# Kernel optimization log

Hardware: AMD Instinct MI355X
Metric: run time of the kernel (lower is better)

The kernel has to match this reference:

```python
import jax, jax.numpy as jnp
import numpy as np

N_SENT = 65536
N_BAGS = 4096
REL_DIM = 768
FLAT_C = 53
GLOBAL_C = 95


def setup_inputs() -> dict:
    key = jax.random.key(0)
    k1, k2, k3, k4, k5 = jax.random.split(key, 5)
    x = jax.random.normal(k1, (N_SENT, REL_DIM), dtype=jnp.float32)
    attention_query = jax.random.randint(k2, (N_SENT, 3), 0, GLOBAL_C, dtype=jnp.int32)
    # strictly increasing interior boundaries -> every bag non-empty
    rng = np.random.RandomState(0)
    interior = np.sort(rng.choice(np.arange(1, N_SENT), N_BAGS - 1, replace=False))
    scope = jnp.asarray(np.concatenate([[0], interior, [N_SENT]]), dtype=jnp.int32)
    # learned params (xavier-like scale for embeddings, normal bias)
    attention_weight = jax.random.normal(k3, (GLOBAL_C, REL_DIM), dtype=jnp.float32) * (2.0 / (GLOBAL_C + REL_DIM)) ** 0.5
    relation_weight = jax.random.normal(k4, (FLAT_C, REL_DIM * 3), dtype=jnp.float32) * (2.0 / (FLAT_C + REL_DIM * 3)) ** 0.5
    bias = jax.random.normal(k5, (FLAT_C,), dtype=jnp.float32)
    return {"x": x, "attention_query": attention_query, "scope": scope,
            "attention_weight": attention_weight, "relation_weight": relation_weight,
            "bias": bias}


def _segment_ids(scope, n):
    # scope: [B+1] offsets; build per-sentence bag id via boundary scatter + cumsum
    marks = jnp.zeros((n,), dtype=jnp.int32).at[scope[1:-1]].add(1)
    return jnp.cumsum(marks)


def reference(x, attention_query, scope, attention_weight, relation_weight, bias):
    n = x.shape[0]
    n_bags = scope.shape[0] - 1
    seg = _segment_ids(scope, n)  # [N]

    # per-layer attention logits: sum(x * attention_emb, -1) for all 3 layers at once
    att = attention_weight[attention_query]                # [N, 3, D]
    logit = jnp.einsum('nd,nld->nl', x, att)               # [N, 3]

    # segment (per-bag) softmax over sentences, per layer
    seg_max = jax.ops.segment_max(logit, seg, num_segments=n_bags)   # [B, 3]
    w = jnp.exp(logit - seg_max[seg])
    denom = jax.ops.segment_sum(w, seg, num_segments=n_bags)         # [B, 3]
    w = w / denom[seg]                                               # [N, 3]

    # weighted sentence aggregation per bag, per layer
    bag = jax.ops.segment_sum(w[:, :, None] * x[:, None, :], seg, num_segments=n_bags)  # [B, 3, D]

    stack_logits_layers = jnp.transpose(bag, (1, 0, 2))    # [3, B, D]
    logits_total = bag.reshape(n_bags, -1)                 # [B, 3*D] == cat(layer0, layer1, layer2)
    # dropout in eval mode (identity); global_ratio > 0 -> compute probs
    probs = logits_total @ relation_weight.T + bias        # [B, FLAT_C]
    return (stack_logits_layers, logits_total, probs)
```

## Files before the change

kernel.cpp:

```cpp
#include <hip/hip_runtime.h>
#include <math.h>

#define NSENT 65536
#define NBAGS 4096
#define DIM 768
#define D4 192
#define FLATC 53
#define CPAD 64
#define KTOT 2304
#define K4 576
#define CHUNK 512

typedef short bf16x8 __attribute__((ext_vector_type(8)));
typedef float f32x4 __attribute__((ext_vector_type(4)));

__device__ __forceinline__ float wsum(float v) {
#pragma unroll
  for (int o = 32; o; o >>= 1) v += __shfl_xor(v, o);
  return v;
}
__device__ __forceinline__ float wmax(float v) {
#pragma unroll
  for (int o = 32; o; o >>= 1) v = fmaxf(v, __shfl_xor(v, o));
  return v;
}
__device__ __forceinline__ float dot4(float4 a, float4 b) {
  return a.x * b.x + a.y * b.y + a.z * b.z + a.w * b.w;
}
__device__ __forceinline__ unsigned short f2bf(float f) {
  unsigned int u = __float_as_uint(f);
  return (unsigned short)((u + 0x7FFFu + ((u >> 16) & 1u)) >> 16);
}

__global__ __launch_bounds__(256) void logit_kernel(
    const float* __restrict__ x, const int* __restrict__ q,
    const float* __restrict__ aw, float* __restrict__ lgout) {
  const int wid = (blockIdx.x * 256 + threadIdx.x) >> 6;
  const int lane = threadIdx.x & 63;
  const int n0 = wid * 2;
  if (n0 >= NSENT) return;
  const int n1 = n0 + 1;

  const int qa0 = q[3 * n0 + 0], qa1 = q[3 * n0 + 1], qa2 = q[3 * n0 + 2];
  const int qb0 = q[3 * n1 + 0], qb1 = q[3 * n1 + 1], qb2 = q[3 * n1 + 2];

  const float4* __restrict__ X4 = (const float4*)x;
  const float4* __restrict__ AW4 = (const float4*)aw;
  const float4* xr0 = X4 + (size_t)n0 * D4;
  const float4* xr1 = X4 + (size_t)n1 * D4;
  const float4* A00 = AW4 + (size_t)qa0 * D4;
  const float4* A01 = AW4 + (size_t)qa1 * D4;
  const float4* A02 = AW4 + (size_t)qa2 * D4;
  const float4* A10 = AW4 + (size_t)qb0 * D4;
  const float4* A11 = AW4 + (size_t)qb1 * D4;
  const float4* A12 = AW4 + (size_t)qb2 * D4;

  float p00 = 0.f, p01 = 0.f, p02 = 0.f;
  float p10 = 0.f, p11 = 0.f, p12 = 0.f;
#pragma unroll
  for (int j = 0; j < 3; j++) {
    const int idx = lane + 64 * j;
    const float4 x0 = xr0[idx];
    const float4 x1 = xr1[idx];
    p00 += dot4(x0, A00[idx]);
    p01 += dot4(x0, A01[idx]);
    p02 += dot4(x0, A02[idx]);
    p10 += dot4(x1, A10[idx]);
    p11 += dot4(x1, A11[idx]);
    p12 += dot4(x1, A12[idx]);
  }
  p00 = wsum(p00); p01 = wsum(p01); p02 = wsum(p02);
  p10 = wsum(p10); p11 = wsum(p11); p12 = wsum(p12);
  if (lane == 0) {
    lgout[3 * n0 + 0] = p00;
    lgout[3 * n0 + 1] = p01;
    lgout[3 * n0 + 2] = p02;
    lgout[3 * n1 + 0] = p10;
    lgout[3 * n1 + 1] = p11;
    lgout[3 * n1 + 2] = p12;
  }
}

__global__ __launch_bounds__(192) void bag_sum(
    const float* __restrict__ x, const float* __restrict__ lgin,
    const int* __restrict__ scope, float* __restrict__ out,
    unsigned short* __restrict__ lt16) {
  const int b = blockIdx.x;
  const int s0 = scope[b];
  const int s1 = scope[b + 1];
  const int len = s1 - s0;
  const int tid = threadIdx.x;
  const int wave = tid >> 6;
  const int lane = tid & 63;

  __shared__ float lg[CHUNK][3];
  __shared__ float sm[3], se[3];

  float m[3] = {-INFINITY, -INFINITY, -INFINITY};
  float dsum[3] = {0.f, 0.f, 0.f};
  float4 acc[3];
#pragma unroll
  for (int l = 0; l < 3; l++) acc[l] = make_float4(0.f, 0.f, 0.f, 0.f);

  const float4* __restrict__ X4 = (const float4*)x;

  for (int cs = 0; cs < len; cs += CHUNK) {
    const int clen = min(CHUNK, len - cs);

    for (int idx = tid; idx < 3 * clen; idx += 192)
      ((float*)lg)[idx] = lgin[(size_t)(s0 + cs) * 3 + idx];
    __syncthreads();

    {
      const int l = wave;
      float cm = -INFINITY;
      for (int i = lane; i < clen; i += 64) cm = fmaxf(cm, lg[i][l]);
      cm = wmax(cm);
      const float mn = fmaxf(m[l], cm);
      float es = 0.f;
      for (int i = lane; i < clen; i += 64) {
        const float e = __expf(lg[i][l] - mn);
        es += e;
        lg[i][l] = e;
      }
      es = wsum(es);
      if (lane == 0) {
        sm[l] = mn;
        se[l] = es;
      }
    }
    __syncthreads();

#pragma unroll
    for (int l = 0; l < 3; l++) {
      const float mn = sm[l];
      const float sc = __expf(m[l] - mn);
      m[l] = mn;
      dsum[l] = dsum[l] * sc + se[l];
      acc[l].x *= sc; acc[l].y *= sc; acc[l].z *= sc; acc[l].w *= sc;
    }

    {
      int i = 0;
      for (; i + 4 <= clen; i += 4) {
        float4 xv[4];
        float w0[4], w1[4], w2[4];
#pragma unroll
        for (int j = 0; j < 4; j++) {
          xv[j] = X4[(size_t)(s0 + cs + i + j) * D4 + tid];
          w0[j] = lg[i + j][0];
          w1[j] = lg[i + j][1];
          w2[j] = lg[i + j][2];
        }
#pragma unroll
        for (int j = 0; j < 4; j++) {
          acc[0].x += w0[j] * xv[j].x; acc[0].y += w0[j] * xv[j].y;
          acc[0].z += w0[j] * xv[j].z; acc[0].w += w0[j] * xv[j].w;
          acc[1].x += w1[j] * xv[j].x; acc[1].y += w1[j] * xv[j].y;
          acc[1].z += w1[j] * xv[j].z; acc[1].w += w1[j] * xv[j].w;
          acc[2].x += w2[j] * xv[j].x; acc[2].y += w2[j] * xv[j].y;
          acc[2].z += w2[j] * xv[j].z; acc[2].w += w2[j] * xv[j].w;
        }
      }
      for (; i < clen; i++) {
        const float a0 = lg[i][0], a1 = lg[i][1], a2 = lg[i][2];
        const float4 xv = X4[(size_t)(s0 + cs + i) * D4 + tid];
        acc[0].x += a0 * xv.x; acc[0].y += a0 * xv.y; acc[0].z += a0 * xv.z; acc[0].w += a0 * xv.w;
        acc[1].x += a1 * xv.x; acc[1].y += a1 * xv.y; acc[1].z += a1 * xv.z; acc[1].w += a1 * xv.w;
        acc[2].x += a2 * xv.x; acc[2].y += a2 * xv.y; acc[2].z += a2 * xv.z; acc[2].w += a2 * xv.w;
      }
    }
    __syncthreads();
  }

  float4* o0 = (float4*)out;
  float4* o1 = (float4*)(out + (size_t)3 * NBAGS * DIM);
  ushort4* l16 = (ushort4*)(lt16 + (size_t)b * KTOT);
#pragma unroll
  for (int l = 0; l < 3; l++) {
    const float inv = (dsum[l] > 0.f) ? (1.f / dsum[l]) : 0.f;
    float4 v = acc[l];
    v.x *= inv; v.y *= inv; v.z *= inv; v.w *= inv;
    o0[((size_t)l * NBAGS + b) * D4 + tid] = v;
    o1[(size_t)b * K4 + l * D4 + tid] = v;
    ushort4 h;
    h.x = f2bf(v.x); h.y = f2bf(v.y); h.z = f2bf(v.z); h.w = f2bf(v.w);
    l16[l * D4 + tid] = h;
  }
}

__global__ __launch_bounds__(256) void rwcvt(const float* __restrict__ rw,
                                             unsigned short* __restrict__ rw16) {
  const int idx = blockIdx.x * 256 + threadIdx.x;
  if (idx < CPAD * KTOT) {
    const int row = idx / KTOT;
    const float v = (row < FLATC) ? rw[idx] : 0.f;
    rw16[idx] = f2bf(v);
  }
}

__global__ __launch_bounds__(256) void probs_mfma(
    const unsigned short* __restrict__ lt16,
    const unsigned short* __restrict__ rw16,
    const float* __restrict__ bias, float* __restrict__ outp) {
  const int wv = threadIdx.x >> 6;
  const int lane = threadIdx.x & 63;
  const int r = lane & 15;
  const int kg = lane >> 4;
  const int bagbase = blockIdx.x * 64 + wv * 16;

  f32x4 acc[4];
#pragma unroll
  for (int ct = 0; ct < 4; ct++) acc[ct] = (f32x4){0.f, 0.f, 0.f, 0.f};

  const unsigned short* ap = lt16 + (size_t)(bagbase + r) * KTOT + kg * 8;
  const unsigned short* bp[4];
#pragma unroll
  for (int ct = 0; ct < 4; ct++)
    bp[ct] = rw16 + (size_t)(ct * 16 + r) * KTOT + kg * 8;

  for (int k = 0; k < KTOT; k += 32) {
    const bf16x8 a = *(const bf16x8*)(ap + k);
#pragma unroll
    for (int ct = 0; ct < 4; ct++) {
      const bf16x8 bb = *(const bf16x8*)(bp[ct] + k);
      acc[ct] = __builtin_amdgcn_mfma_f32_16x16x32_bf16(a, bb, acc[ct], 0, 0, 0);
    }
  }

#pragma unroll
  for (int ct = 0; ct < 4; ct++) {
    const int col = ct * 16 + r;
    if (col < FLATC) {
      const float bv = bias[col];
#pragma unroll
      for (int reg = 0; reg < 4; reg++) {
        const int bag = bagbase + kg * 4 + reg;
        outp[(size_t)bag * FLATC + col] = acc[ct][reg] + bv;
      }
    }
  }
}

extern "C" void kernel_launch(void* const* d_in, const int* in_sizes, int n_in,
                              void* d_out, int out_size, void* d_ws,
                              size_t ws_size, hipStream_t stream) {
  const float* x = (const float*)d_in[0];
  const int* aq = (const int*)d_in[1];
  const int* scope = (const int*)d_in[2];
  const float* aw = (const float*)d_in[3];
  const float* rw = (const float*)d_in[4];
  const float* bias = (const float*)d_in[5];
  float* out = (float*)d_out;

  unsigned short* lt16 = (unsigned short*)d_ws;
  unsigned short* rw16 = lt16 + (size_t)NBAGS * KTOT;
  float* lgbuf = (float*)(rw16 + (size_t)CPAD * KTOT);

  hipLaunchKernelGGL(logit_kernel, dim3(NSENT / 2 / 4), dim3(256), 0, stream,
                     x, aq, aw, lgbuf);
  hipLaunchKernelGGL(bag_sum, dim3(NBAGS), dim3(192), 0, stream, x, lgbuf,
                     scope, out, lt16);
  hipLaunchKernelGGL(rwcvt, dim3((CPAD * KTOT + 255) / 256), dim3(256), 0,
                     stream, rw, rw16);

  float* probs = out + (size_t)3 * NBAGS * DIM + (size_t)NBAGS * KTOT;
  hipLaunchKernelGGL(probs_mfma, dim3(NBAGS / 64), dim3(256), 0, stream, lt16,
                     rw16, bias, probs);
}
```

Before: 162.0 us.

## Compute attention logits as dense bf16 MFMA GEMM against all classes, then gather

```diff
diff --git a/kernel.cpp b/kernel.cpp
--- a/kernel.cpp
+++ b/kernel.cpp
@@ -1,4 +1,5 @@
 #include <hip/hip_runtime.h>
+#include <hip/hip_bf16.h>
 #include <math.h>
 
 #define NSENT 65536
@@ -7,9 +8,11 @@
 #define D4 192
 #define FLATC 53
 #define CPAD 64
+#define GCLS 96
 #define KTOT 2304
 #define K4 576
 #define CHUNK 512
+#define MROWS 128
 
 typedef short bf16x8 __attribute__((ext_vector_type(8)));
 typedef float f32x4 __attribute__((ext_vector_type(4)));
@@ -24,67 +27,78 @@
   for (int o = 32; o; o >>= 1) v = fmaxf(v, __shfl_xor(v, o));
   return v;
 }
-__device__ __forceinline__ float dot4(float4 a, float4 b) {
-  return a.x * b.x + a.y * b.y + a.z * b.z + a.w * b.w;
-}
 __device__ __forceinline__ unsigned short f2bf(float f) {
-  unsigned int u = __float_as_uint(f);
-  return (unsigned short)((u + 0x7FFFu + ((u >> 16) & 1u)) >> 16);
-}
-
-__global__ __launch_bounds__(256) void logit_kernel(
-    const float* __restrict__ x, const int* __restrict__ q,
-    const float* __restrict__ aw, float* __restrict__ lgout) {
-  const int wid = (blockIdx.x * 256 + threadIdx.x) >> 6;
+  union { __hip_bfloat16 b; unsigned short s; } cv;
+  cv.b = __float2bfloat16(f);
+  return cv.s;
+}
+__device__ __forceinline__ bf16x8 cvt8(float4 lo, float4 hi) {
+  union { bf16x8 v; unsigned short s[8]; } u;
+  u.s[0] = f2bf(lo.x); u.s[1] = f2bf(lo.y); u.s[2] = f2bf(lo.z); u.s[3] = f2bf(lo.w);
+  u.s[4] = f2bf(hi.x); u.s[5] = f2bf(hi.y); u.s[6] = f2bf(hi.z); u.s[7] = f2bf(hi.w);
+  return u.v;
+}
+
+__global__ __launch_bounds__(256) void cvt_weights(
+    const float* __restrict__ aw, const float* __restrict__ rw,
+    unsigned short* __restrict__ aw16, unsigned short* __restrict__ rw16) {
+  const int idx = blockIdx.x * 256 + threadIdx.x;
+  const int NAW = GCLS * DIM;
+  if (idx < NAW) {
+    const int row = idx / DIM;
+    aw16[idx] = f2bf(row < 95 ? aw[idx] : 0.f);
+  } else if (idx < NAW + CPAD * KTOT) {
+    const int j = idx - NAW;
+    const int row = j / KTOT;
+    rw16[j] = f2bf(row < FLATC ? rw[j] : 0.f);
+  }
+}
+
+__global__ __launch_bounds__(256) void logit_gemm(
+    const float* __restrict__ x, const unsigned short* __restrict__ aw16,
+    float* __restrict__ L) {
+  const int wv = threadIdx.x >> 6;
   const int lane = threadIdx.x & 63;
-  const int n0 = wid * 2;
-  if (n0 >= NSENT) return;
-  const int n1 = n0 + 1;
-
-  const int qa0 = q[3 * n0 + 0], qa1 = q[3 * n0 + 1], qa2 = q[3 * n0 + 2];
-  const int qb0 = q[3 * n1 + 0], qb1 = q[3 * n1 + 1], qb2 = q[3 * n1 + 2];
-
-  const float4* __restrict__ X4 = (const float4*)x;
-  const float4* __restrict__ AW4 = (const float4*)aw;
-  const float4* xr0 = X4 + (size_t)n0 * D4;
-  const float4* xr1 = X4 + (size_t)n1 * D4;
-  const float4* A00 = AW4 + (size_t)qa0 * D4;
-  const float4* A01 = AW4 + (size_t)qa1 * D4;
-  const float4* A02 = AW4 + (size_t)qa2 * D4;
-  const float4* A10 = AW4 + (size_t)qb0 * D4;
-  const float4* A11 = AW4 + (size_t)qb1 * D4;
-  const float4* A12 = AW4 + (size_t)qb2 * D4;
-
-  float p00 = 0.f, p01 = 0.f, p02 = 0.f;
-  float p10 = 0.f, p11 = 0.f, p12 = 0.f;
-#pragma unroll
-  for (int j = 0; j < 3; j++) {
-    const int idx = lane + 64 * j;
-    const float4 x0 = xr0[idx];
-    const float4 x1 = xr1[idx];
-    p00 += dot4(x0, A00[idx]);
-    p01 += dot4(x0, A01[idx]);
-    p02 += dot4(x0, A02[idx]);
-    p10 += dot4(x1, A10[idx]);
-    p11 += dot4(x1, A11[idx]);
-    p12 += dot4(x1, A12[idx]);
-  }
-  p00 = wsum(p00); p01 = wsum(p01); p02 = wsum(p02);
-  p10 = wsum(p10); p11 = wsum(p11); p12 = wsum(p12);
-  if (lane == 0) {
-    lgout[3 * n0 + 0] = p00;
-    lgout[3 * n0 + 1] = p01;
-    lgout[3 * n0 + 2] = p02;
-    lgout[3 * n1 + 0] = p10;
-    lgout[3 * n1 + 1] = p11;
-    lgout[3 * n1 + 2] = p12;
-  }
+  const int r = lane & 15;
+  const int kg = lane >> 4;
+  const int m0 = blockIdx.x * MROWS + wv * 32;
+
+  f32x4 acc[2][6];
+#pragma unroll
+  for (int t = 0; t < 2; t++)
+#pragma unroll
+    for (int ct = 0; ct < 6; ct++) acc[t][ct] = (f32x4){0.f, 0.f, 0.f, 0.f};
+
+  const float4* xp0 = (const float4*)(x + (size_t)(m0 + r) * DIM) + kg * 2;
+  const float4* xp1 = (const float4*)(x + (size_t)(m0 + 16 + r) * DIM) + kg * 2;
+  const unsigned short* bwp = aw16 + (size_t)r * DIM + kg * 8;
+
+  for (int k = 0; k < DIM; k += 32) {
+    const int f4 = k >> 2;
+    const bf16x8 a0 = cvt8(xp0[f4], xp0[f4 + 1]);
+    const bf16x8 a1 = cvt8(xp1[f4], xp1[f4 + 1]);
+#pragma unroll
+    for (int ct = 0; ct < 6; ct++) {
+      const bf16x8 b = *(const bf16x8*)(bwp + (size_t)ct * 16 * DIM + k);
+      acc[0][ct] = __builtin_amdgcn_mfma_f32_16x16x32_bf16(a0, b, acc[0][ct], 0, 0, 0);
+      acc[1][ct] = __builtin_amdgcn_mfma_f32_16x16x32_bf16(a1, b, acc[1][ct], 0, 0, 0);
+    }
+  }
+
+#pragma unroll
+  for (int t = 0; t < 2; t++)
+#pragma unroll
+    for (int ct = 0; ct < 6; ct++)
+#pragma unroll
+      for (int reg = 0; reg < 4; reg++)
+        L[(size_t)(m0 + t * 16 + kg * 4 + reg) * GCLS + ct * 16 + r] =
+            acc[t][ct][reg];
 }
 
 __global__ __launch_bounds__(192) void bag_sum(
-    const float* __restrict__ x, const float* __restrict__ lgin,
-    const int* __restrict__ scope, float* __restrict__ out,
-    unsigned short* __restrict__ lt16) {
+    const float* __restrict__ x, const float* __restrict__ L,
+    const int* __restrict__ q, const int* __restrict__ scope,
+    float* __restrict__ out, unsigned short* __restrict__ lt16) {
   const int b = blockIdx.x;
   const int s0 = scope[b];
   const int s1 = scope[b + 1];
@@ -107,8 +121,12 @@
   for (int cs = 0; cs < len; cs += CHUNK) {
     const int clen = min(CHUNK, len - cs);
 
-    for (int idx = tid; idx < 3 * clen; idx += 192)
-      ((float*)lg)[idx] = lgin[(size_t)(s0 + cs) * 3 + idx];
+    for (int idx = tid; idx < 3 * clen; idx += 192) {
+      const int i = idx / 3;
+      const int l = idx - 3 * i;
+      const int n = s0 + cs + i;
+      ((float*)lg)[idx] = L[(size_t)n * GCLS + q[3 * n + l]];
+    }
     __syncthreads();
 
     {
@@ -124,10 +142,7 @@
         lg[i][l] = e;
       }
       es = wsum(es);
-      if (lane == 0) {
-        sm[l] = mn;
-        se[l] = es;
-      }
+      if (lane == 0) { sm[l] = mn; se[l] = es; }
     }
     __syncthreads();
 
@@ -186,16 +201,6 @@
     ushort4 h;
     h.x = f2bf(v.x); h.y = f2bf(v.y); h.z = f2bf(v.z); h.w = f2bf(v.w);
     l16[l * D4 + tid] = h;
-  }
-}
-
-__global__ __launch_bounds__(256) void rwcvt(const float* __restrict__ rw,
-                                             unsigned short* __restrict__ rw16) {
-  const int idx = blockIdx.x * 256 + threadIdx.x;
-  if (idx < CPAD * KTOT) {
-    const int row = idx / KTOT;
-    const float v = (row < FLATC) ? rw[idx] : 0.f;
-    rw16[idx] = f2bf(v);
   }
 }
 
@@ -255,14 +260,16 @@
 
   unsigned short* lt16 = (unsigned short*)d_ws;
   unsigned short* rw16 = lt16 + (size_t)NBAGS * KTOT;
-  float* lgbuf = (float*)(rw16 + (size_t)CPAD * KTOT);
-
-  hipLaunchKernelGGL(logit_kernel, dim3(NSENT / 2 / 4), dim3(256), 0, stream,
-                     x, aq, aw, lgbuf);
-  hipLaunchKernelGGL(bag_sum, dim3(NBAGS), dim3(192), 0, stream, x, lgbuf,
+  unsigned short* aw16 = rw16 + (size_t)CPAD * KTOT;
+  float* L = (float*)(aw16 + (size_t)GCLS * DIM);
+
+  const int ncvt = GCLS * DIM + CPAD * KTOT;
+  hipLaunchKernelGGL(cvt_weights, dim3((ncvt + 255) / 256), dim3(256), 0,
+                     stream, aw, rw, aw16, rw16);
+  hipLaunchKernelGGL(logit_gemm, dim3(NSENT / MROWS), dim3(256), 0, stream, x,
+                     aw16, L);
+  hipLaunchKernelGGL(bag_sum, dim3(NBAGS), dim3(192), 0, stream, x, L, aq,
                      scope, out, lt16);
-  hipLaunchKernelGGL(rwcvt, dim3((CPAD * KTOT + 255) / 256), dim3(256), 0,
-                     stream, rw, rw16);
 
   float* probs = out + (size_t)3 * NBAGS * DIM + (size_t)NBAGS * KTOT;
   hipLaunchKernelGGL(probs_mfma, dim3(NBAGS / 64), dim3(256), 0, stream, lt16,
```

Result: slower. 219.1 us (+35.2%).

## Split bag softmax into stats kernel and one-wave-per-bag aggregation

Applied to the files above, without the earlier changes.

```diff
diff --git a/kernel.cpp b/kernel.cpp
--- a/kernel.cpp
+++ b/kernel.cpp
@@ -1,4 +1,5 @@
 #include <hip/hip_runtime.h>
+#include <hip/hip_bf16.h>
 #include <math.h>
 
 #define NSENT 65536
@@ -9,7 +10,6 @@
 #define CPAD 64
 #define KTOT 2304
 #define K4 576
-#define CHUNK 512
 
 typedef short bf16x8 __attribute__((ext_vector_type(8)));
 typedef float f32x4 __attribute__((ext_vector_type(4)));
@@ -28,8 +28,18 @@
   return a.x * b.x + a.y * b.y + a.z * b.z + a.w * b.w;
 }
 __device__ __forceinline__ unsigned short f2bf(float f) {
-  unsigned int u = __float_as_uint(f);
-  return (unsigned short)((u + 0x7FFFu + ((u >> 16) & 1u)) >> 16);
+  union { __hip_bfloat16 b; unsigned short s; } cv;
+  cv.b = __float2bfloat16(f);
+  return cv.s;
+}
+
+__global__ __launch_bounds__(256) void rwcvt(const float* __restrict__ rw,
+                                             unsigned short* __restrict__ rw16) {
+  const int idx = blockIdx.x * 256 + threadIdx.x;
+  if (idx < CPAD * KTOT) {
+    const int row = idx / KTOT;
+    rw16[idx] = f2bf(row < FLATC ? rw[idx] : 0.f);
+  }
 }
 
 __global__ __launch_bounds__(256) void logit_kernel(
@@ -81,96 +91,102 @@
   }
 }
 
-__global__ __launch_bounds__(192) void bag_sum(
-    const float* __restrict__ x, const float* __restrict__ lgin,
-    const int* __restrict__ scope, float* __restrict__ out,
-    unsigned short* __restrict__ lt16) {
-  const int b = blockIdx.x;
+__global__ __launch_bounds__(256) void bagstats(
+    const float* __restrict__ lg, const int* __restrict__ scope,
+    float* __restrict__ wexp, float* __restrict__ dinv) {
+  const int b = blockIdx.x * 4 + (threadIdx.x >> 6);
+  const int lane = threadIdx.x & 63;
   const int s0 = scope[b];
   const int s1 = scope[b + 1];
   const int len = s1 - s0;
-  const int tid = threadIdx.x;
-  const int wave = tid >> 6;
-  const int lane = tid & 63;
-
-  __shared__ float lg[CHUNK][3];
-  __shared__ float sm[3], se[3];
-
-  float m[3] = {-INFINITY, -INFINITY, -INFINITY};
-  float dsum[3] = {0.f, 0.f, 0.f};
-  float4 acc[3];
-#pragma unroll
-  for (int l = 0; l < 3; l++) acc[l] = make_float4(0.f, 0.f, 0.f, 0.f);
+
+  float mx0 = -INFINITY, mx1 = -INFINITY, mx2 = -INFINITY;
+  for (int i = lane; i < len; i += 64) {
+    const int n = s0 + i;
+    mx0 = fmaxf(mx0, lg[3 * n + 0]);
+    mx1 = fmaxf(mx1, lg[3 * n + 1]);
+    mx2 = fmaxf(mx2, lg[3 * n + 2]);
+  }
+  mx0 = wmax(mx0); mx1 = wmax(mx1); mx2 = wmax(mx2);
+
+  float s0e = 0.f, s1e = 0.f, s2e = 0.f;
+  for (int i = lane; i < len; i += 64) {
+    const int n = s0 + i;
+    const float e0 = __expf(lg[3 * n + 0] - mx0);
+    const float e1 = __expf(lg[3 * n + 1] - mx1);
+    const float e2 = __expf(lg[3 * n + 2] - mx2);
+    wexp[3 * n + 0] = e0;
+    wexp[3 * n + 1] = e1;
+    wexp[3 * n + 2] = e2;
+    s0e += e0; s1e += e1; s2e += e2;
+  }
+  s0e = wsum(s0e); s1e = wsum(s1e); s2e = wsum(s2e);
+  if (lane == 0) {
+    dinv[3 * b + 0] = 1.f / s0e;
+    dinv[3 * b + 1] = 1.f / s1e;
+    dinv[3 * b + 2] = 1.f / s2e;
+  }
+}
+
+__global__ __launch_bounds__(256, 4) void agg(
+    const float* __restrict__ x, const float* __restrict__ wexp,
+    const float* __restrict__ dinv, const int* __restrict__ scope,
+    float* __restrict__ out, unsigned short* __restrict__ lt16) {
+  const int b = blockIdx.x * 4 + (threadIdx.x >> 6);
+  const int lane = threadIdx.x & 63;
+  const int s0 = scope[b];
+  const int s1 = scope[b + 1];
+  const int len = s1 - s0;
 
   const float4* __restrict__ X4 = (const float4*)x;
 
-  for (int cs = 0; cs < len; cs += CHUNK) {
-    const int clen = min(CHUNK, len - cs);
-
-    for (int idx = tid; idx < 3 * clen; idx += 192)
-      ((float*)lg)[idx] = lgin[(size_t)(s0 + cs) * 3 + idx];
-    __syncthreads();
-
-    {
-      const int l = wave;
-      float cm = -INFINITY;
-      for (int i = lane; i < clen; i += 64) cm = fmaxf(cm, lg[i][l]);
-      cm = wmax(cm);
-      const float mn = fmaxf(m[l], cm);
-      float es = 0.f;
-      for (int i = lane; i < clen; i += 64) {
-        const float e = __expf(lg[i][l] - mn);
-        es += e;
-        lg[i][l] = e;
-      }
-      es = wsum(es);
-      if (lane == 0) {
-        sm[l] = mn;
-        se[l] = es;
-      }
-    }
-    __syncthreads();
-
-#pragma unroll
-    for (int l = 0; l < 3; l++) {
-      const float mn = sm[l];
-      const float sc = __expf(m[l] - mn);
-      m[l] = mn;
-      dsum[l] = dsum[l] * sc + se[l];
-      acc[l].x *= sc; acc[l].y *= sc; acc[l].z *= sc; acc[l].w *= sc;
-    }
-
-    {
-      int i = 0;
-      for (; i + 4 <= clen; i += 4) {
-        float4 xv[4];
-        float w0[4], w1[4], w2[4];
-#pragma unroll
-        for (int j = 0; j < 4; j++) {
-          xv[j] = X4[(size_t)(s0 + cs + i + j) * D4 + tid];
-          w0[j] = lg[i + j][0];
-          w1[j] = lg[i + j][1];
-          w2[j] = lg[i + j][2];
+  f32x4 acc[3][3];
+#pragma unroll
+  for (int l = 0; l < 3; l++)
+#pragma unroll
+    for (int k = 0; k < 3; k++) acc[l][k] = (f32x4){0.f, 0.f, 0.f, 0.f};
+
+  int i = 0;
+  for (; i + 4 <= len; i += 4) {
+    float w[4][3];
+    float4 xv[4][3];
+#pragma unroll
+    for (int j = 0; j < 4; j++) {
+      const int n = s0 + i + j;
+      w[j][0] = wexp[3 * n + 0];
+      w[j][1] = wexp[3 * n + 1];
+      w[j][2] = wexp[3 * n + 2];
+#pragma unroll
+      for (int k = 0; k < 3; k++)
+        xv[j][k] = X4[(size_t)n * D4 + lane + 64 * k];
+    }
+#pragma unroll
+    for (int j = 0; j < 4; j++)
+#pragma unroll
+      for (int l = 0; l < 3; l++)
+#pragma unroll
+        for (int k = 0; k < 3; k++) {
+          acc[l][k][0] += w[j][l] * xv[j][k].x;
+          acc[l][k][1] += w[j][l] * xv[j][k].y;
+          acc[l][k][2] += w[j][l] * xv[j][k].z;
+          acc[l][k][3] += w[j][l] * xv[j][k].w;
         }
-#pragma unroll
-        for (int j = 0; j < 4; j++) {
-          acc[0].x += w0[j] * xv[j].x; acc[0].y += w0[j] * xv[j].y;
-          acc[0].z += w0[j] * xv[j].z; acc[0].w += w0[j] * xv[j].w;
-          acc[1].x += w1[j] * xv[j].x; acc[1].y += w1[j] * xv[j].y;
-          acc[1].z += w1[j] * xv[j].z; acc[1].w += w1[j] * xv[j].w;
-          acc[2].x += w2[j] * xv[j].x; acc[2].y += w2[j] * xv[j].y;
-          acc[2].z += w2[j] * xv[j].z; acc[2].w += w2[j] * xv[j].w;
-        }
-      }
-      for (; i < clen; i++) {
-        const float a0 = lg[i][0], a1 = lg[i][1], a2 = lg[i][2];
-        const float4 xv = X4[(size_t)(s0 + cs + i) * D4 + tid];
-        acc[0].x += a0 * xv.x; acc[0].y += a0 * xv.y; acc[0].z += a0 * xv.z; acc[0].w += a0 * xv.w;
-        acc[1].x += a1 * xv.x; acc[1].y += a1 * xv.y; acc[1].z += a1 * xv.z; acc[1].w += a1 * xv.w;
-        acc[2].x += a2 * xv.x; acc[2].y += a2 * xv.y; acc[2].z += a2 * xv.z; acc[2].w += a2 * xv.w;
-      }
-    }
-    __syncthreads();
+  }
+  for (; i < len; i++) {
+    const int n = s0 + i;
+    const float w0 = wexp[3 * n + 0];
+    const float w1 = wexp[3 * n + 1];
+    const float w2 = wexp[3 * n + 2];
+#pragma unroll
+    for (int k = 0; k < 3; k++) {
+      const float4 xv = X4[(size_t)n * D4 + lane + 64 * k];
+      acc[0][k][0] += w0 * xv.x; acc[0][k][1] += w0 * xv.y;
+      acc[0][k][2] += w0 * xv.z; acc[0][k][3] += w0 * xv.w;
+      acc[1][k][0] += w1 * xv.x; acc[1][k][1] += w1 * xv.y;
+      acc[1][k][2] += w1 * xv.z; acc[1][k][3] += w1 * xv.w;
+      acc[2][k][0] += w2 * xv.x; acc[2][k][1] += w2 * xv.y;
+      acc[2][k][2] += w2 * xv.z; acc[2][k][3] += w2 * xv.w;
+    }
   }
 
   float4* o0 = (float4*)out;
@@ -178,24 +194,21 @@
   ushort4* l16 = (ushort4*)(lt16 + (size_t)b * KTOT);
 #pragma unroll
   for (int l = 0; l < 3; l++) {
-    const float inv = (dsum[l] > 0.f) ? (1.f / dsum[l]) : 0.f;
-    float4 v = acc[l];
-    v.x *= inv; v.y *= inv; v.z *= inv; v.w *= inv;
-    o0[((size_t)l * NBAGS + b) * D4 + tid] = v;
-    o1[(size_t)b * K4 + l * D4 + tid] = v;
-    ushort4 h;
-    h.x = f2bf(v.x); h.y = f2bf(v.y); h.z = f2bf(v.z); h.w = f2bf(v.w);
-    l16[l * D4 + tid] = h;
-  }
-}
-
-__global__ __launch_bounds__(256) void rwcvt(const float* __restrict__ rw,
-                                             unsigned short* __restrict__ rw16) {
-  const int idx = blockIdx.x * 256 + threadIdx.x;
-  if (idx < CPAD * KTOT) {
-    const int row = idx / KTOT;
-    const float v = (row < FLATC) ? rw[idx] : 0.f;
-    rw16[idx] = f2bf(v);
+    const float di = dinv[3 * b + l];
+#pragma unroll
+    for (int k = 0; k < 3; k++) {
+      const int c = lane + 64 * k;
+      float4 v;
+      v.x = acc[l][k][0] * di;
+      v.y = acc[l][k][1] * di;
+      v.z = acc[l][k][2] * di;
+      v.w = acc[l][k][3] * di;
+      o0[((size_t)l * NBAGS + b) * D4 + c] = v;
+      o1[(size_t)b * K4 + l * D4 + c] = v;
+      ushort4 h;
+      h.x = f2bf(v.x); h.y = f2bf(v.y); h.z = f2bf(v.z); h.w = f2bf(v.w);
+      l16[l * D4 + c] = h;
+    }
   }
 }
 
@@ -256,13 +269,17 @@
   unsigned short* lt16 = (unsigned short*)d_ws;
   unsigned short* rw16 = lt16 + (size_t)NBAGS * KTOT;
   float* lgbuf = (float*)(rw16 + (size_t)CPAD * KTOT);
-
+  float* wexp = lgbuf + (size_t)NSENT * 3;
+  float* dinv = wexp + (size_t)NSENT * 3;
+
+  hipLaunchKernelGGL(rwcvt, dim3((CPAD * KTOT + 255) / 256), dim3(256), 0,
+                     stream, rw, rw16);
   hipLaunchKernelGGL(logit_kernel, dim3(NSENT / 2 / 4), dim3(256), 0, stream,
                      x, aq, aw, lgbuf);
-  hipLaunchKernelGGL(bag_sum, dim3(NBAGS), dim3(192), 0, stream, x, lgbuf,
-                     scope, out, lt16);
-  hipLaunchKernelGGL(rwcvt, dim3((CPAD * KTOT + 255) / 256), dim3(256), 0,
-                     stream, rw, rw16);
+  hipLaunchKernelGGL(bagstats, dim3(NBAGS / 4), dim3(256), 0, stream, lgbuf,
+                     scope, wexp, dinv);
+  hipLaunchKernelGGL(agg, dim3(NBAGS / 4), dim3(256), 0, stream, x, wexp,
+                     dinv, scope, out, lt16);
 
   float* probs = out + (size_t)3 * NBAGS * DIM + (size_t)NBAGS * KTOT;
   hipLaunchKernelGGL(probs_mfma, dim3(NBAGS / 64), dim3(256), 0, stream, lt16,
```

Measured after the change: 295.5 us. 1.82x slower.
